# Kernel optimization log

Hardware: AMD Instinct MI355X
Metric: run time of the kernel (lower is better)

The kernel has to match this reference:

```python
import jax, jax.numpy as jnp
import numpy as np
from jax.scipy.special import logsumexp


def setup_inputs() -> dict:
    key = jax.random.key(0)
    B, C, H, W = 2, 32, 128, 128
    sizes = [(H, W)] + [(H // 2, W // 2)] * 4
    ks = iter(jax.random.split(key, 32))
    inp = {}
    for t, (hh, ww) in enumerate(sizes):
        inp[f"unary_h{t}"] = jax.random.normal(next(ks), (B, C, hh, ww), jnp.float32)
        inp[f"unary_v{t}"] = jax.random.normal(next(ks), (B, C, hh, ww), jnp.float32)
        inp[f"pairwise_h{t}"] = 0.1 * jax.random.normal(next(ks), (B, C, C, hh, ww - 1), jnp.float32)
        inp[f"pairwise_v{t}"] = 0.1 * jax.random.normal(next(ks), (B, C, C, hh - 1, ww), jnp.float32)
    inp["gamma"] = jnp.ones((1,), jnp.float32)
    return inp


def _chain_marginals(unary, pairwise, gamma):
    """Entropy-smoothed max-product marginals along the LAST axis.
    unary: [B,C,L,T], pairwise: [B,C,C,L,T-1] (pairwise[b,i,j,l,t] couples state i at t with j at t+1).
    Returns soft marginals [B,C,L,T] (softmax over C per position)."""
    u = jnp.transpose(unary, (3, 0, 2, 1))        # [T,B,L,C]
    pw = jnp.transpose(pairwise, (4, 0, 3, 1, 2))  # [T-1,B,L,C,C]
    inv_g = 1.0 / gamma

    def fwd_step(f, xs):
        u_t, pw_t = xs
        f_new = u_t + gamma * logsumexp(f[..., :, None] * inv_g + pw_t * inv_g, axis=-2)
        return f_new, f_new

    _, f_rest = jax.lax.scan(fwd_step, u[0], (u[1:], pw))
    f = jnp.concatenate([u[:1], f_rest], axis=0)

    def bwd_step(bb, xs):
        u_t, pw_t = xs
        b_new = u_t + gamma * logsumexp(bb[..., None, :] * inv_g + pw_t * inv_g, axis=-1)
        return b_new, b_new

    _, b_rest = jax.lax.scan(bwd_step, u[-1], (u[:-1][::-1], pw[::-1]))
    b = jnp.concatenate([u[-1:], b_rest], axis=0)[::-1]

    marg = jax.nn.softmax((f + b - u) * inv_g, axis=-1)  # [T,B,L,C]
    return jnp.transpose(marg, (1, 3, 2, 0))             # [B,C,L,T]


def _dp_pair(uh, uv, ph, pv, g):
    # horizontal chains (along W) with unary_h, vertical chains (along H) with unary_v
    mh = _chain_marginals(uh, ph, g)
    mv = _chain_marginals(uv.swapaxes(2, 3), pv.swapaxes(3, 4), g).swapaxes(2, 3)
    return mh, mv


def _scatter_up(m, stride, i, j, H, W):
    # max_unpool2d with the structured indices: m[y,x] -> (i + y*stride, j + x*stride), then crop/pad to (H,W)
    b, c, h_, w_ = m.shape
    up = jnp.zeros((b, c, h_ * stride, w_ * stride), m.dtype).at[:, :, i::stride, j::stride].set(m)
    up = up[:, :, :H, :W]
    ph, pw = H - up.shape[2], W - up.shape[3]
    if ph > 0 or pw > 0:
        up = jnp.pad(up, ((0, 0), (0, 0), (0, max(ph, 0)), (0, max(pw, 0))))
    return up


def reference(unary_h0, unary_h1, unary_h2, unary_h3, unary_h4,
              unary_v0, unary_v1, unary_v2, unary_v3, unary_v4,
              pairwise_h0, pairwise_h1, pairwise_h2, pairwise_h3, pairwise_h4,
              pairwise_v0, pairwise_v1, pairwise_v2, pairwise_v3, pairwise_v4,
              gamma):
    uh = [unary_h0, unary_h1, unary_h2, unary_h3, unary_h4]
    uv = [unary_v0, unary_v1, unary_v2, unary_v3, unary_v4]
    ph = [pairwise_h0, pairwise_h1, pairwise_h2, pairwise_h3, pairwise_h4]
    pv = [pairwise_v0, pairwise_v1, pairwise_v2, pairwise_v3, pairwise_v4]
    g = jnp.clip(gamma.reshape(()), 0.01)  # learned gamma, clamped min 0.01

    H, W = uh[0].shape[2], uh[0].shape[3]
    alpha = 1.0 / W if W > H else 1.0 / H

    mh0, mv0 = _dp_pair(uh[0], uv[0], ph[0], pv[0], g)
    marg_hs, marg_vs = [mh0], [mv0]
    mh_acc, mv_acc = mh0, mv0

    stride, cnt = 2, 1  # step_size = 1 default -> one extra scale with a 2x2 shifted grid
    for i in range(stride):
        for j in range(stride):
            m_h, m_v = _dp_pair(uh[cnt], uv[cnt], ph[cnt], pv[cnt], g)
            marg_hs.append(m_h)
            marg_vs.append(m_v)
            mh_acc = mh_acc + _scatter_up(m_h, stride, i, j, H, W)
            mv_acc = mv_acc + _scatter_up(m_v, stride, i, j, H, W)
            cnt += 1

    num_pairwise_terms = 2
    avg = (mh_acc + mv_acc) / (num_pairwise_terms * 2)

    new_uh0 = uh[0] - alpha * (marg_hs[0] - avg)
    new_uv0 = uv[0] - alpha * (marg_vs[0] - avg)
    # fine-scale unary updates (computed for faithfulness; gradients flow through avg)
    cnt = 1
    new_uh_fine, new_uv_fine = [], []
    for i in range(stride):
        for j in range(stride):
            new_uh_fine.append(uh[cnt] - alpha * (marg_hs[cnt] - avg[:, :, i::stride, j::stride]))
            new_uv_fine.append(uv[cnt] - alpha * (marg_vs[cnt] - avg[:, :, i::stride, j::stride]))
            cnt += 1

    main = jnp.stack([new_uh0, new_uv0, mh_acc, mv_acc], axis=0)  # [4,B,C,H,W]
    return main
```

## Files before the change

### kernel.cpp

```cpp
#include <hip/hip_runtime.h>
#include <stdint.h>

#define TC 2
#define CHUNK_BYTES 4096
#define CHUNK_F4 256

typedef float floatx4 __attribute__((ext_vector_type(4)));

static __device__ __forceinline__ float softmax32_l2(float z)
{
  float zm = z;
  zm = fmaxf(zm, __shfl_xor(zm, 16));
  zm = fmaxf(zm, __shfl_xor(zm, 8));
  zm = fmaxf(zm, __shfl_xor(zm, 4));
  zm = fmaxf(zm, __shfl_xor(zm, 2));
  zm = fmaxf(zm, __shfl_xor(zm, 1));
  float p = exp2f(z - zm);
  float ps = p;
  ps += __shfl_xor(ps, 16);
  ps += __shfl_xor(ps, 8);
  ps += __shfl_xor(ps, 4);
  ps += __shfl_xor(ps, 2);
  ps += __shfl_xor(ps, 1);
  return p / ps;
}

static __device__ __forceinline__ uint32_t pkbf(float a, float b)
{
  uint32_t ua = __float_as_uint(a), ub = __float_as_uint(b);
  ua = (ua + 0x7FFFu + ((ua >> 16) & 1u)) >> 16;
  ub = (ub + 0x7FFFu + ((ub >> 16) & 1u)) & 0xFFFF0000u;
  return ua | ub;
}

static __device__ __forceinline__ float rfl(float x)
{
  return __int_as_float(__builtin_amdgcn_readfirstlane(__float_as_int(x)));
}

#define RLF(x, i) __int_as_float(__builtin_amdgcn_readlane(__float_as_int(x), (i)))

static __device__ __forceinline__ float dot16_rl(const float* w, float e, int h)
{
  float a0, a1, a2, a3, b0, b1, b2, b3;
  a0 = w[0]  * RLF(e, 0)  + w[1]  * RLF(e, 1);
  a1 = w[2]  * RLF(e, 2)  + w[3]  * RLF(e, 3);
  a2 = w[4]  * RLF(e, 4)  + w[5]  * RLF(e, 5);
  a3 = w[6]  * RLF(e, 6)  + w[7]  * RLF(e, 7);
  a0 += w[8]  * RLF(e, 8)  + w[9]  * RLF(e, 9);
  a1 += w[10] * RLF(e, 10) + w[11] * RLF(e, 11);
  a2 += w[12] * RLF(e, 12) + w[13] * RLF(e, 13);
  a3 += w[14] * RLF(e, 14) + w[15] * RLF(e, 15);
  float dlo = (a0 + a1) + (a2 + a3);
  b0 = w[0]  * RLF(e, 16) + w[1]  * RLF(e, 17);
  b1 = w[2]  * RLF(e, 18) + w[3]  * RLF(e, 19);
  b2 = w[4]  * RLF(e, 20) + w[5]  * RLF(e, 21);
  b3 = w[6]  * RLF(e, 22) + w[7]  * RLF(e, 23);
  b0 += w[8]  * RLF(e, 24) + w[9]  * RLF(e, 25);
  b1 += w[10] * RLF(e, 26) + w[11] * RLF(e, 27);
  b2 += w[12] * RLF(e, 28) + w[13] * RLF(e, 29);
  b3 += w[14] * RLF(e, 30) + w[15] * RLF(e, 31);
  float dhi = (b0 + b1) + (b2 + b3);
  return h ? dhi : dlo;
}

struct TSeg { const float* pw; uint16_t* PT; int L, Tt, Tpad, fStride, Xtot, dirV, blockBase, nx, ny; };
struct TTable { TSeg s[10]; int nseg; };
struct USeg { const float* U; float* Ut; int fs, nx, ny, L, T, dirV, blockBase; };
struct UTable { USeg s[10]; int nseg; };
struct DSeg { const uint16_t* PT; const float* Ut; float* F; float* B; int chainBase, T, Tt, Tpad; };
struct DTable { DSeg s[10]; int nseg; };
struct MSeg { const float* F; const float* B; const float* Ut; float* out; int L, T, dirV, blockBase, nrx, nfx; };
struct MTable { MSeg s[10]; int nseg; };

template <typename T_>
static void zeroTbl(T_* p)
{
  unsigned char* c = (unsigned char*)p;
  for (size_t i = 0; i < sizeof(T_); i++) c[i] = 0;
}

static __device__ void tp_run(const TTable& tbl, int r0blk, int tid, float igl2, unsigned char* ldsraw)
{
  typedef uint16_t (*TileT)[128];
  TileT tile = (TileT)ldsraw;
  int bid = r0blk;
  int k = 0;
  for (int q = 1; q < tbl.nseg; q++) if (bid >= tbl.s[q].blockBase) k = q;
  const TSeg& sg = tbl.s[k];
  int r = bid - sg.blockBase;
  int jg = r & 7; r >>= 3;
  int w = r % sg.nx; int tmp = r / sg.nx;
  int fixed = tmp % sg.ny;
  int b = tmp / sg.ny;
  int j0 = jg * 4;
  int g = fixed * sg.fStride;
  int a = g & 31;
  int xbase = w * 128 - a;
  if (xbase >= sg.Xtot) return;
  int kx = tid & 31, psub = tid >> 5;
  int pstride = sg.L * sg.Tt;
  int clampMax = 2048 * pstride - 4;
  int jthr = j0 + (psub & 3);
  int swj = (jthr >> 1) & 3;
  int gp0 = ((psub >> 2) << 5) + jthr;
  int idx0 = ((b << 10) + gp0) * pstride + (g - a) + (w << 7) + (kx << 2);
  const float* pw = sg.pw;
  #pragma unroll
  for (int hp = 0; hp < 2; hp++) {
    floatx4 st[8];
    #pragma unroll
    for (int q = 0; q < 8; q++) {
      int batch = hp * 8 + q;
      int idx = idx0 + batch * (pstride << 6);
      idx = idx > clampMax ? clampMax : idx;
      st[q] = __builtin_nontemporal_load((const floatx4*)(pw + idx));
    }
    #pragma unroll
    for (int q = 0; q < 8; q++) {
      int batch = hp * 8 + q;
      int i = 2 * batch + (psub >> 2);
      int sw = swj ^ (((i >> 3) & 3) << 2);
      int pl = batch * 8 + psub;
      uint32_t pk0 = pkbf(exp2f(st[q].x * igl2), exp2f(st[q].y * igl2));
      uint32_t pk1 = pkbf(exp2f(st[q].z * igl2), exp2f(st[q].w * igl2));
      if (sw & 1) { uint32_t tswp = pk0; pk0 = pk1; pk1 = tswp; }
      *(uint2*)(ldsraw + pl * 256 + 8 * (kx ^ (sw >> 1))) = make_uint2(pk0, pk1);
    }
  }
  __syncthreads();
  uint32_t* PTd = (uint32_t*)sg.PT;
  #pragma unroll
  for (int w8 = 0; w8 < 8; w8++) {
    int gidx = w8 * 256 + tid;
    int xs = gidx >> 4;
    int q = gidx & 15;
    int xv = xbase + xs;
    if (xv < 0 || xv >= sg.Xtot) continue;
    int jl = q >> 2, j = j0 + jl;
    int perm3 = (j >> 1) & 7;
    int swjW = (j >> 1) & 3;
    uint32_t pk[4];
    #pragma unroll
    for (int e = 0; e < 4; e++) {
      int wd = ((q & 3) << 2) + e;
      int pos = wd >> 1, pr = wd & 1;
      int i0 = ((pos ^ perm3) << 2) + pr * 2;
      int sw = swjW ^ (((i0 >> 3) & 3) << 2);
      int c = (xs >> 1) ^ sw;
      int u16c = (c << 1) | (xs & 1);
      int rr0 = (i0 << 2) + jl;
      uint32_t v0 = tile[rr0][u16c];
      uint32_t v1 = tile[rr0 + 4][u16c];
      pk[e] = v0 | (v1 << 16);
    }
    int chain, tsl;
    if (sg.dirV) { chain = b * sg.Xtot + xv; tsl = fixed; }
    else         { chain = b * sg.ny + fixed; tsl = xv; }
    *(uint4*)&PTd[((size_t)chain * sg.Tpad + tsl) * 512 + j * 16 + (q & 3) * 4] =
        make_uint4(pk[0], pk[1], pk[2], pk[3]);
  }
}

static __device__ void ut_run(const UTable& tbl, int r0blk, int tid, float igl2, unsigned char* ldsraw)
{
  typedef float (*UTileT)[33];
  UTileT tile = (UTileT)ldsraw;
  int bid = r0blk;
  int k = 0;
  for (int q = 1; q < tbl.nseg; q++) if (bid >= tbl.s[q].blockBase) k = q;
  const USeg& sg = tbl.s[k];
  int r = bid - sg.blockBase;
  int bx = r % sg.nx; int tmp = r / sg.nx;
  int fixed = tmp % sg.ny;
  int b = tmp / sg.ny;
  size_t LT = (size_t)sg.L * sg.T;
  int x0 = bx * 32;
  int xx = tid & 31;
  #pragma unroll
  for (int it = 0; it < 4; it++) {
    int c = (tid >> 5) + it * 8;
    tile[xx][c] = sg.U[(size_t)b * 32 * LT + (size_t)c * LT + (size_t)fixed * sg.fs + x0 + xx];
  }
  __syncthreads();
  int xw = tid >> 3;
  int ci = (tid & 7) * 4;
  int chain = sg.dirV ? b * sg.L + x0 + xw : b * sg.L + fixed;
  int tIdx  = sg.dirV ? fixed : x0 + xw;
  float4 vv = make_float4(tile[xw][ci] * igl2, tile[xw][ci + 1] * igl2,
                          tile[xw][ci + 2] * igl2, tile[xw][ci + 3] * igl2);
  *(float4*)&sg.Ut[((size_t)chain * sg.T + tIdx) * 32 + ci] = vv;
}

static __device__ void dp_run(const DTable& tbl, int nDP, int dpBid, int tid256, unsigned char* ldsAll)
{
  int wid = tid256 >> 6;
  unsigned char* lds = ldsAll + wid * (2 * CHUNK_BYTES + 1024);
  float* f_out = (float*)(lds + 2 * CHUNK_BYTES);
  int gw = dpBid * 4 + wid;
  if (gw >= 2 * nDP) return;
  int isB = (gw >= nDP) ? 1 : 0;
  int bid = gw - isB * nDP;
  int k = 0;
  for (int q = 1; q < tbl.nseg; q++) if (bid >= tbl.s[q].chainBase) k = q;
  const DSeg& sg = tbl.s[k];
  int chain = bid - sg.chainBase;
  int T = sg.T, Tt = sg.Tt;
  int tid = tid256 & 63, j = tid & 31, h = tid >> 5;
  const float* Utc = sg.Ut + (size_t)chain * T * 32;
  float* Oc = (isB ? sg.B : sg.F) + (size_t)chain * T * 32;
  const float4* src = (const float4*)(sg.PT + (size_t)chain * sg.Tpad * 1024);
  int nch = sg.Tpad / TC;
  int perm3 = (j >> 1) & 7;
  float4 stg[4];
  float uCur[TC], uNxt[TC];
  if (!isB) {
    float cur = Utc[j];
    if (h == 0) f_out[j] = cur;
    float eCur = exp2f(cur - rfl(cur));
    #pragma unroll
    for (int ss = 0; ss < TC; ss++) {
      int t = ss + 1; t = t > Tt ? Tt : t;
      uCur[ss] = Utc[(size_t)t * 32 + j];
    }
    #pragma unroll
    for (int q = 0; q < 4; q++) stg[q] = src[q * 64 + tid];
    int buf = 0;
    for (int ch = 0; ch < nch; ch++) {
      float4* dst = (float4*)(lds + buf * CHUNK_BYTES);
      #pragma unroll
      for (int q = 0; q < 4; q++) dst[q * 64 + tid] = stg[q];
      if (ch + 1 < nch) {
        const float4* s2 = src + (size_t)(ch + 1) * CHUNK_F4;
        #pragma unroll
        for (int q = 0; q < 4; q++) stg[q] = s2[q * 64 + tid];
        #pragma unroll
        for (int ss = 0; ss < TC; ss++) {
          int t = (ch + 1) * TC + ss + 1; t = t > Tt ? Tt : t;
          uNxt[ss] = Utc[(size_t)t * 32 + j];
        }
      }
      #pragma unroll
      for (int ss = 0; ss < TC; ss++) {
        int s = ch * TC + ss;
        if (s >= Tt) break;
        int t = s + 1;
        const uint32_t* sl = (const uint32_t*)(lds + buf * CHUNK_BYTES + ss * 2048);
        float w[16];
        #pragma unroll
        for (int rr = 0; rr < 4; rr++) {
          int pos = (4 * h + rr) ^ perm3;
          uint2 dv = *(const uint2*)&sl[j * 16 + pos * 2];
          w[rr * 4 + 0] = __uint_as_float(dv.x << 16);
          w[rr * 4 + 1] = __uint_as_float(dv.x & 0xFFFF0000u);
          w[rr * 4 + 2] = __uint_as_float(dv.y << 16);
          w[rr * 4 + 3] = __uint_as_float(dv.y & 0xFFFF0000u);
        }
        float dot = dot16_rl(w, eCur, h);
        float dot2 = dot + __shfl_xor(dot, 32);
        cur = uCur[ss] + __log2f(dot2);
        if (h == 0) f_out[(t & 7) * 32 + j] = cur;
        eCur = exp2f(cur - rfl(cur));
        if ((t & 7) == 7) {
          float4 vv = *(float4*)&f_out[tid * 4];
          *(float4*)&Oc[(size_t)(t - 7) * 32 + tid * 4] = vv;
        }
      }
      #pragma unroll
      for (int ss = 0; ss < TC; ss++) uCur[ss] = uNxt[ss];
      buf ^= 1;
    }
  } else {
    int p2i = j >> 2, pri = (j >> 1) & 1, loi = j & 1;
    float cur = Utc[(size_t)(T - 1) * 32 + j];
    if (h == 0) f_out[7 * 32 + j] = cur;
    float eCur = exp2f(cur - rfl(cur));
    #pragma unroll
    for (int ss = 0; ss < TC; ss++) {
      int s = (nch - 1) * TC + ss; s = s > Tt - 1 ? Tt - 1 : s; s = s < 0 ? 0 : s;
      uCur[ss] = Utc[(size_t)s * 32 + j];
    }
    {
      const float4* s2 = src + (size_t)(nch - 1) * CHUNK_F4;
      #pragma unroll
      for (int q = 0; q < 4; q++) stg[q] = s2[q * 64 + tid];
    }
    int buf = 0;
    for (int ch = nch - 1; ch >= 0; ch--) {
      float4* dst = (float4*)(lds + buf * CHUNK_BYTES);
      #pragma unroll
      for (int q = 0; q < 4; q++) dst[q * 64 + tid] = stg[q];
      if (ch > 0) {
        const float4* s2 = src + (size_t)(ch - 1) * CHUNK_F4;
        #pragma unroll
        for (int q = 0; q < 4; q++) stg[q] = s2[q * 64 + tid];
        #pragma unroll
        for (int ss = 0; ss < TC; ss++) {
          int s = (ch - 1) * TC + ss; s = s > Tt - 1 ? Tt - 1 : s; s = s < 0 ? 0 : s;
          uNxt[ss] = Utc[(size_t)s * 32 + j];
        }
      }
      #pragma unroll
      for (int ss = TC - 1; ss >= 0; ss--) {
        int s = ch * TC + ss;
        if (s >= Tt) continue;
        const uint16_t* row16 = (const uint16_t*)(lds + buf * CHUNK_BYTES + ss * 2048);
        float w[16];
        #pragma unroll
        for (int jj = 0; jj < 16; jj++) {
          int u16idx = (16 * h + jj) * 32 + ((p2i ^ (jj >> 1)) * 2 + pri) * 2 + loi;
          w[jj] = __uint_as_float((uint32_t)row16[u16idx] << 16);
        }
        float dot = dot16_rl(w, eCur, h);
        float dot2 = dot + __shfl_xor(dot, 32);
        cur = uCur[ss] + __log2f(dot2);
        if (h == 0) f_out[(s & 7) * 32 + j] = cur;
        eCur = exp2f(cur - rfl(cur));
        if ((s & 7) == 0) {
          float4 vv = *(float4*)&f_out[tid * 4];
          *(float4*)&Oc[(size_t)s * 32 + tid * 4] = vv;
        }
      }
      #pragma unroll
      for (int ss = 0; ss < TC; ss++) uCur[ss] = uNxt[ss];
      buf ^= 1;
    }
  }
}

__global__ __launch_bounds__(256) void k_fused(TTable tt, DTable dt, int dpB, int nDP,
                                               UTable ut, int uB, const float* __restrict__ gamma)
{
  __shared__ __align__(16) unsigned char lds[4 * (2 * CHUNK_BYTES + 1024)];
  int bid = blockIdx.x, tid = threadIdx.x;
  if (bid < dpB) {
    dp_run(dt, nDP, bid, tid, lds);
  } else if (bid < dpB + uB) {
    float igl2 = 1.4426950408889634f / fmaxf(gamma[0], 0.01f);
    ut_run(ut, bid - dpB, tid, igl2, lds);
  } else {
    float igl2 = 1.4426950408889634f / fmaxf(gamma[0], 0.01f);
    tp_run(tt, bid - dpB - uB, tid, igl2, lds);
  }
}

__global__ __launch_bounds__(256) void k_marg_all(MTable tbl)
{
  __shared__ float sm[32][33];
  int bid = blockIdx.x;
  int k = 0;
  for (int q = 1; q < tbl.nseg; q++) if (bid >= tbl.s[q].blockBase) k = q;
  MSeg sg = tbl.s[k];
  int r = bid - sg.blockBase;
  int rx = r % sg.nrx; int tmp = r / sg.nrx;
  int fx = tmp % sg.nfx; int b = tmp / sg.nfx;
  int tid = threadIdx.x;
  int c = tid & 31;
  int L = sg.L, T = sg.T;
  size_t LT = (size_t)L * T;
  int RA = sg.dirV ? L : T;
  int r0 = rx * 32;
  #pragma unroll
  for (int pass = 0; pass < 4; pass++) {
    int rr = (tid >> 5) + pass * 8;
    int rowAxis = r0 + rr;
    int chain = sg.dirV ? b * L + rowAxis : b * L + fx;
    int t = sg.dirV ? fx : rowAxis;
    size_t idx = ((size_t)chain * T + t) * 32 + c;
    float z = sg.F[idx] + sg.B[idx] - sg.Ut[idx];
    sm[rr][c] = softmax32_l2(z);
  }
  __syncthreads();
  int cc = tid >> 3;
  int xl = (tid & 7) * 4;
  size_t obase = (size_t)b * 32 * LT + (size_t)fx * RA + r0;
  float4 vv = make_float4(sm[xl][cc], sm[xl + 1][cc], sm[xl + 2][cc], sm[xl + 3][cc]);
  *(float4*)&sg.out[obase + (size_t)cc * LT + xl] = vv;
}

__global__ __launch_bounds__(256) void k_combine(
    const float* __restrict__ uh0, const float* __restrict__ uv0,
    const float* __restrict__ MB, float* __restrict__ out)
{
  int t4 = blockIdx.x * 256 + threadIdx.x;
  int base = t4 * 4;
  int x = base & 127, y = (base >> 7) & 127;
  int bc = base >> 14;
  float4 mh0 = *(const float4*)&MB[base];
  float4 mv0 = *(const float4*)&MB[1048576 + base];
  int ce = 1 + ((y & 1) << 1);
  int coff = bc * 4096 + ((y >> 1) << 6) + (x >> 1);
  const float* cbE = MB + 2097152 + (size_t)(ce - 1) * 524288;
  const float* cbO = cbE + 524288;
  float2 mhcE = *(const float2*)&cbE[coff];
  float2 mhcO = *(const float2*)&cbO[coff];
  float2 mvcE = *(const float2*)&cbE[262144 + coff];
  float2 mvcO = *(const float2*)&cbO[262144 + coff];
  float4 u_h = *(const float4*)&uh0[base];
  float4 u_v = *(const float4*)&uv0[base];
  float mh[4] = {mh0.x, mh0.y, mh0.z, mh0.w};
  float mv[4] = {mv0.x, mv0.y, mv0.z, mv0.w};
  float uh[4] = {u_h.x, u_h.y, u_h.z, u_h.w};
  float uv[4] = {u_v.x, u_v.y, u_v.z, u_v.w};
  float mhc[4] = {mhcE.x, mhcO.x, mhcE.y, mhcO.y};
  float mvc[4] = {mvcE.x, mvcO.x, mvcE.y, mvcO.y};
  float o0[4], o1[4], o2[4], o3[4];
  const float A = 0.0078125f;
  #pragma unroll
  for (int e = 0; e < 4; e++) {
    float mha = mh[e] + mhc[e], mva = mv[e] + mvc[e];
    float avg = (mha + mva) * 0.25f;
    o0[e] = uh[e] - A * (mh[e] - avg);
    o1[e] = uv[e] - A * (mv[e] - avg);
    o2[e] = mha; o3[e] = mva;
  }
  *(float4*)&out[base]           = make_float4(o0[0], o0[1], o0[2], o0[3]);
  *(float4*)&out[1048576 + base] = make_float4(o1[0], o1[1], o1[2], o1[3]);
  *(float4*)&out[2097152 + base] = make_float4(o2[0], o2[1], o2[2], o2[3]);
  *(float4*)&out[3145728 + base] = make_float4(o3[0], o3[1], o3[2], o3[3]);
}

static void fill_tseg(TSeg& t, const float* pw, uint16_t* PT, int L, int T, int dirV, int blockBase)
{
  int Tt = T - 1;
  t.pw = pw; t.PT = PT;
  t.L = L; t.Tt = Tt; t.Tpad = T;
  t.fStride = dirV ? L : Tt;
  t.Xtot = dirV ? L : Tt;
  t.dirV = dirV;
  int pad = (t.fStride & 31) ? 31 : 0;
  t.nx = (t.Xtot + pad + 127) / 128;
  t.ny = dirV ? Tt : L;
  t.blockBase = blockBase;
}

extern "C" void kernel_launch(void* const* d_in, const int* in_sizes, int n_in,
                              void* d_out, int out_size, void* d_ws, size_t ws_size,
                              hipStream_t stream)
{
  (void)in_sizes; (void)n_in; (void)out_size; (void)ws_size;
  const float* gamma = (const float*)d_in[20];
  unsigned char* ws = (unsigned char*)d_ws;

  int segL[10], segT[10];
  const float* segPW[10]; const float* segUU[10];
  size_t segMG[10];
  for (int lvl = 0; lvl < 5; lvl++) {
    int H = lvl ? 64 : 128, W = H;
    int si = lvl * 2;
    segL[si] = H; segT[si] = W;
    segPW[si] = (const float*)d_in[lvl * 4 + 2];
    segUU[si] = (const float*)d_in[lvl * 4 + 0];
    segL[si + 1] = W; segT[si + 1] = H;
    segPW[si + 1] = (const float*)d_in[lvl * 4 + 3];
    segUU[si + 1] = (const float*)d_in[lvl * 4 + 1];
    if (lvl == 0) { segMG[0] = 0; segMG[1] = 1048576; }
    else { segMG[si] = 2097152 + (size_t)(lvl - 1) * 524288; segMG[si + 1] = segMG[si] + 262144; }
  }

  uint16_t* PT_A = (uint16_t*)ws;
  uint16_t* PT_B = (uint16_t*)(ws + 134217728ull);
  float* MARG = (float*)ws;
  float* F0  = (float*)(ws + 268435456ull);
  float* B0  = (float*)(ws + 285212672ull);
  float* Ut0 = (float*)(ws + 301989888ull);

  size_t fuOffOf[10];
  {
    size_t fuOff = 0;
    for (int s = 0; s < 10; s++) {
      fuOffOf[s] = fuOff;
      fuOff += (size_t)(2 * segL[s]) * segT[s] * 32;
    }
  }

  UTable ut; zeroTbl(&ut); ut.nseg = 10;
  int uB = 0;
  for (int s = 0; s < 10; s++) {
    int dirV = s & 1;
    USeg& u = ut.s[s];
    u.U = segUU[s]; u.Ut = Ut0 + fuOffOf[s];
    u.fs = dirV ? segL[s] : segT[s];
    u.nx = (dirV ? segL[s] : segT[s]) / 32;
    u.ny = dirV ? segT[s] : segL[s];
    u.L = segL[s]; u.T = segT[s]; u.dirV = dirV;
    u.blockBase = uB;
    uB += u.nx * u.ny * 2;
  }

  TTable tt0, tt1; DTable dt0, dt1;
  zeroTbl(&tt0); zeroTbl(&tt1); zeroTbl(&dt0); zeroTbl(&dt1);
  int tB0 = 0, tB1 = 0, cB0 = 0, cB1 = 0;
  {
    size_t ptOff = 0;
    tt0.nseg = 2; dt0.nseg = 2;
    for (int s = 0; s < 2; s++) {
      int dirV = s & 1;
      int L = segL[s], T = segT[s];
      int chains = 2 * L;
      fill_tseg(tt0.s[s], segPW[s], PT_A + ptOff, L, T, dirV, tB0);
      tB0 += 2 * tt0.s[s].ny * tt0.s[s].nx * 8;
      DSeg& d = dt0.s[s];
      d.PT = PT_A + ptOff; d.Ut = Ut0 + fuOffOf[s];
      d.F = F0 + fuOffOf[s]; d.B = B0 + fuOffOf[s];
      d.chainBase = cB0; d.T = T; d.Tt = T - 1; d.Tpad = T;
      cB0 += chains;
      ptOff += (size_t)chains * T * 1024;
    }
  }
  {
    size_t ptOff = 0;
    tt1.nseg = 8; dt1.nseg = 8;
    for (int s = 2; s < 10; s++) {
      int i = s - 2;
      int dirV = s & 1;
      int L = segL[s], T = segT[s];
      int chains = 2 * L;
      fill_tseg(tt1.s[i], segPW[s], PT_B + ptOff, L, T, dirV, tB1);
      tB1 += 2 * tt1.s[i].ny * tt1.s[i].nx * 8;
      DSeg& d = dt1.s[i];
      d.PT = PT_B + ptOff; d.Ut = Ut0 + fuOffOf[s];
      d.F = F0 + fuOffOf[s]; d.B = B0 + fuOffOf[s];
      d.chainBase = cB1; d.T = T; d.Tt = T - 1; d.Tpad = T;
      cB1 += chains;
      ptOff += (size_t)chains * T * 1024;
    }
  }
  int dpB0 = (2 * cB0 + 3) / 4;
  int dpB1 = (2 * cB1 + 3) / 4;
  DTable dtEmpty; zeroTbl(&dtEmpty); dtEmpty.nseg = 1;
  UTable utEmpty; zeroTbl(&utEmpty); utEmpty.nseg = 1;
  TTable ttEmpty; zeroTbl(&ttEmpty); ttEmpty.nseg = 1;

  k_fused<<<uB + tB0, 256, 0, stream>>>(tt0, dtEmpty, 0, 0, ut, uB, gamma);
  k_fused<<<dpB0 + tB1, 256, 0, stream>>>(tt1, dt0, dpB0, cB0, utEmpty, 0, gamma);
  k_fused<<<dpB1, 256, 0, stream>>>(ttEmpty, dt1, dpB1, cB1, utEmpty, 0, gamma);

  MTable mt; zeroTbl(&mt); mt.nseg = 10;
  int mB = 0;
  for (int s = 0; s < 10; s++) {
    int dirV = s & 1;
    MSeg& m = mt.s[s];
    m.F = F0 + fuOffOf[s]; m.B = B0 + fuOffOf[s]; m.Ut = Ut0 + fuOffOf[s];
    m.out = MARG + segMG[s];
    m.L = segL[s]; m.T = segT[s]; m.dirV = dirV;
    m.blockBase = mB;
    m.nrx = (dirV ? segL[s] : segT[s]) / 32;
    m.nfx = dirV ? segT[s] : segL[s];
    mB += 2 * m.nfx * m.nrx;
  }
  k_marg_all<<<mB, 256, 0, stream>>>(mt);
  k_combine<<<1024, 256, 0, stream>>>((const float*)d_in[0], (const float*)d_in[1],
                                      MARG, (float*)d_out);
}
```

Baseline: 379.2 us.

## Reorder launch schedule so coarse-level DP overlaps fine-level transpose and marginals

Reorders the three fused launches so the transpose and DP for the four coarse levels run first. The level-0 transpose now overlaps coarse DP, and level-0 DP overlaps the coarse marginal softmax, which moves into the fused kernel as an mg_run branch. The DP wavefronts get raised scheduling priority via s_setprio so they are not starved by the co-resident blocks. MARG moves to the PT_B region to avoid aliasing PT_A, which is still live during level-0 DP. The risk is contention between co-scheduled blocks and a different critical path.

Measured after the change: 387.0 us. 1.02x slower.

```diff
diff --git a/kernel.cpp b/kernel.cpp
--- a/kernel.cpp
+++ b/kernel.cpp
@@ -192,6 +192,40 @@
   *(float4*)&sg.Ut[((size_t)chain * sg.T + tIdx) * 32 + ci] = vv;
 }
 
+static __device__ void mg_run(const MTable& tbl, int r0blk, int tid, unsigned char* ldsraw)
+{
+  typedef float (*SmT)[33];
+  SmT sm = (SmT)ldsraw;
+  int bid = r0blk;
+  int k = 0;
+  for (int q = 1; q < tbl.nseg; q++) if (bid >= tbl.s[q].blockBase) k = q;
+  const MSeg& sg = tbl.s[k];
+  int r = bid - sg.blockBase;
+  int rx = r % sg.nrx; int tmp = r / sg.nrx;
+  int fx = tmp % sg.nfx; int b = tmp / sg.nfx;
+  int c = tid & 31;
+  int L = sg.L, T = sg.T;
+  size_t LT = (size_t)L * T;
+  int RA = sg.dirV ? L : T;
+  int r0 = rx * 32;
+  #pragma unroll
+  for (int pass = 0; pass < 4; pass++) {
+    int rr = (tid >> 5) + pass * 8;
+    int rowAxis = r0 + rr;
+    int chain = sg.dirV ? b * L + rowAxis : b * L + fx;
+    int t = sg.dirV ? fx : rowAxis;
+    size_t idx = ((size_t)chain * T + t) * 32 + c;
+    float z = sg.F[idx] + sg.B[idx] - sg.Ut[idx];
+    sm[rr][c] = softmax32_l2(z);
+  }
+  __syncthreads();
+  int cc = tid >> 3;
+  int xl = (tid & 7) * 4;
+  size_t obase = (size_t)b * 32 * LT + (size_t)fx * RA + r0;
+  float4 vv = make_float4(sm[xl][cc], sm[xl + 1][cc], sm[xl + 2][cc], sm[xl + 3][cc]);
+  *(float4*)&sg.out[obase + (size_t)cc * LT + xl] = vv;
+}
+
 static __device__ void dp_run(const DTable& tbl, int nDP, int dpBid, int tid256, unsigned char* ldsAll)
 {
   int wid = tid256 >> 6;
@@ -214,6 +248,7 @@
   int perm3 = (j >> 1) & 7;
   float4 stg[4];
   float uCur[TC], uNxt[TC];
+  __builtin_amdgcn_s_setprio(1);
   if (!isB) {
     float cur = Utc[j];
     if (h == 0) f_out[j] = cur;
@@ -326,10 +361,12 @@
       buf ^= 1;
     }
   }
+  __builtin_amdgcn_s_setprio(0);
 }
 
 __global__ __launch_bounds__(256) void k_fused(TTable tt, DTable dt, int dpB, int nDP,
-                                               UTable ut, int uB, const float* __restrict__ gamma)
+                                               UTable ut, int uB, MTable mt, int mB,
+                                               const float* __restrict__ gamma)
 {
   __shared__ __align__(16) unsigned char lds[4 * (2 * CHUNK_BYTES + 1024)];
   int bid = blockIdx.x, tid = threadIdx.x;
@@ -338,44 +375,18 @@
   } else if (bid < dpB + uB) {
     float igl2 = 1.4426950408889634f / fmaxf(gamma[0], 0.01f);
     ut_run(ut, bid - dpB, tid, igl2, lds);
+  } else if (bid < dpB + uB + mB) {
+    mg_run(mt, bid - dpB - uB, tid, lds);
   } else {
     float igl2 = 1.4426950408889634f / fmaxf(gamma[0], 0.01f);
-    tp_run(tt, bid - dpB - uB, tid, igl2, lds);
+    tp_run(tt, bid - dpB - uB - mB, tid, igl2, lds);
   }
 }
 
 __global__ __launch_bounds__(256) void k_marg_all(MTable tbl)
 {
-  __shared__ float sm[32][33];
-  int bid = blockIdx.x;
-  int k = 0;
-  for (int q = 1; q < tbl.nseg; q++) if (bid >= tbl.s[q].blockBase) k = q;
-  MSeg sg = tbl.s[k];
-  int r = bid - sg.blockBase;
-  int rx = r % sg.nrx; int tmp = r / sg.nrx;
-  int fx = tmp % sg.nfx; int b = tmp / sg.nfx;
-  int tid = threadIdx.x;
-  int c = tid & 31;
-  int L = sg.L, T = sg.T;
-  size_t LT = (size_t)L * T;
-  int RA = sg.dirV ? L : T;
-  int r0 = rx * 32;
-  #pragma unroll
-  for (int pass = 0; pass < 4; pass++) {
-    int rr = (tid >> 5) + pass * 8;
-    int rowAxis = r0 + rr;
-    int chain = sg.dirV ? b * L + rowAxis : b * L + fx;
-    int t = sg.dirV ? fx : rowAxis;
-    size_t idx = ((size_t)chain * T + t) * 32 + c;
-    float z = sg.F[idx] + sg.B[idx] - sg.Ut[idx];
-    sm[rr][c] = softmax32_l2(z);
-  }
-  __syncthreads();
-  int cc = tid >> 3;
-  int xl = (tid & 7) * 4;
-  size_t obase = (size_t)b * 32 * LT + (size_t)fx * RA + r0;
-  float4 vv = make_float4(sm[xl][cc], sm[xl + 1][cc], sm[xl + 2][cc], sm[xl + 3][cc]);
-  *(float4*)&sg.out[obase + (size_t)cc * LT + xl] = vv;
+  __shared__ __align__(16) unsigned char lds[4352];
+  mg_run(tbl, blockIdx.x, threadIdx.x, lds);
 }
 
 __global__ __launch_bounds__(256) void k_combine(
@@ -460,7 +471,7 @@
 
   uint16_t* PT_A = (uint16_t*)ws;
   uint16_t* PT_B = (uint16_t*)(ws + 134217728ull);
-  float* MARG = (float*)ws;
+  float* MARG = (float*)(ws + 134217728ull);
   float* F0  = (float*)(ws + 268435456ull);
   float* B0  = (float*)(ws + 285212672ull);
   float* Ut0 = (float*)(ws + 301989888ull);
@@ -528,28 +539,43 @@
   }
   int dpB0 = (2 * cB0 + 3) / 4;
   int dpB1 = (2 * cB1 + 3) / 4;
+
+  MTable mt19, mt01; zeroTbl(&mt19); zeroTbl(&mt01);
+  mt19.nseg = 8; mt01.nseg = 2;
+  int mB19 = 0, mB01 = 0;
+  for (int s = 2; s < 10; s++) {
+    int i = s - 2;
+    int dirV = s & 1;
+    MSeg& m = mt19.s[i];
+    m.F = F0 + fuOffOf[s]; m.B = B0 + fuOffOf[s]; m.Ut = Ut0 + fuOffOf[s];
+    m.out = MARG + segMG[s];
+    m.L = segL[s]; m.T = segT[s]; m.dirV = dirV;
+    m.blockBase = mB19;
+    m.nrx = (dirV ? segL[s] : segT[s]) / 32;
+    m.nfx = dirV ? segT[s] : segL[s];
+    mB19 += 2 * m.nfx * m.nrx;
+  }
+  for (int s = 0; s < 2; s++) {
+    int dirV = s & 1;
+    MSeg& m = mt01.s[s];
+    m.F = F0 + fuOffOf[s]; m.B = B0 + fuOffOf[s]; m.Ut = Ut0 + fuOffOf[s];
+    m.out = MARG + segMG[s];
+    m.L = segL[s]; m.T = segT[s]; m.dirV = dirV;
+    m.blockBase = mB01;
+    m.nrx = (dirV ? segL[s] : segT[s]) / 32;
+    m.nfx = dirV ? segT[s] : segL[s];
+    mB01 += 2 * m.nfx * m.nrx;
+  }
+
   DTable dtEmpty; zeroTbl(&dtEmpty); dtEmpty.nseg = 1;
   UTable utEmpty; zeroTbl(&utEmpty); utEmpty.nseg = 1;
   TTable ttEmpty; zeroTbl(&ttEmpty); ttEmpty.nseg = 1;
-
-  k_fused<<<uB + tB0, 256, 0, stream>>>(tt0, dtEmpty, 0, 0, ut, uB, gamma);
-  k_fused<<<dpB0 + tB1, 256, 0, stream>>>(tt1, dt0, dpB0, cB0, utEmpty, 0, gamma);
-  k_fused<<<dpB1, 256, 0, stream>>>(ttEmpty, dt1, dpB1, cB1, utEmpty, 0, gamma);
-
-  MTable mt; zeroTbl(&mt); mt.nseg = 10;
-  int mB = 0;
-  for (int s = 0; s < 10; s++) {
-    int dirV = s & 1;
-    MSeg& m = mt.s[s];
-    m.F = F0 + fuOffOf[s]; m.B = B0 + fuOffOf[s]; m.Ut = Ut0 + fuOffOf[s];
-    m.out = MARG + segMG[s];
-    m.L = segL[s]; m.T = segT[s]; m.dirV = dirV;
-    m.blockBase = mB;
-    m.nrx = (dirV ? segL[s] : segT[s]) / 32;
-    m.nfx = dirV ? segT[s] : segL[s];
-    mB += 2 * m.nfx * m.nrx;
-  }
-  k_marg_all<<<mB, 256, 0, stream>>>(mt);
+  MTable mtEmpty; zeroTbl(&mtEmpty); mtEmpty.nseg = 1;
+
+  k_fused<<<uB + tB1, 256, 0, stream>>>(tt1, dtEmpty, 0, 0, ut, uB, mtEmpty, 0, gamma);
+  k_fused<<<dpB1 + tB0, 256, 0, stream>>>(tt0, dt1, dpB1, cB1, utEmpty, 0, mtEmpty, 0, gamma);
+  k_fused<<<dpB0 + mB19, 256, 0, stream>>>(ttEmpty, dt0, dpB0, cB0, utEmpty, 0, mt19, mB19, gamma);
+  k_marg_all<<<mB01, 256, 0, stream>>>(mt01);
   k_combine<<<1024, 256, 0, stream>>>((const float*)d_in[0], (const float*)d_in[1],
                                       MARG, (float*)d_out);
 }
```
